# Kernel optimization log

Hardware: AMD Instinct MI355X
Metric: run time of the kernel (lower is better)

Reference implementation:

```python
import jax, jax.numpy as jnp
import numpy as np

N_SRC = 8192
N_DST = 8192
E = 524288
D = 128
M = 64


def layer_norm(x, g, b, eps=1e-5):
    mu = x.mean(-1, keepdims=True)
    var = ((x - mu) ** 2).mean(-1, keepdims=True)
    return (x - mu) * jax.lax.rsqrt(var + eps) * g + b


def setup_inputs() -> dict:
    key = jax.random.key(0)
    ks = jax.random.split(key, 32)

    def p(k, shape, s=0.02):
        return jax.random.normal(k, shape, jnp.float32) * s

    inp = {
        "src_embed": jax.random.normal(ks[0], (N_SRC, D), jnp.float32),
        "dst_embed": jax.random.normal(ks[1], (N_DST, D), jnp.float32),
        "v_s2d": jax.random.normal(ks[2], (E, M), jnp.float32),
        "v_d2s": jax.random.normal(ks[3], (E, M), jnp.float32),
        "e_s2d_dst": jax.random.randint(ks[4], (E,), 0, N_DST, jnp.int32),
        "e_d2s_dst": jax.random.randint(ks[5], (E,), 0, N_SRC, jnp.int32),
        # node transforms
        "W_src": p(ks[6], (D, D)), "b_src": jnp.zeros((D,), jnp.float32),
        "W_dst": p(ks[7], (D, D)), "b_dst": jnp.zeros((D,), jnp.float32),
        # edge-message transforms
        "W_sm": p(ks[8], (M, D)), "b_sm": jnp.zeros((D,), jnp.float32),
        "W_dm": p(ks[9], (M, D)), "b_dm": jnp.zeros((D,), jnp.float32),
        # apply_row: LNLayer (Linear+LayerNorm) then Linear
        "row_W1": p(ks[10], (D, D)), "row_b1": jnp.zeros((D,), jnp.float32),
        "row_g": jnp.ones((D,), jnp.float32), "row_beta": jnp.zeros((D,), jnp.float32),
        "row_W2": p(ks[11], (D, D)), "row_b2": jnp.zeros((D,), jnp.float32),
        # apply_col
        "col_W1": p(ks[12], (D, D)), "col_b1": jnp.zeros((D,), jnp.float32),
        "col_g": jnp.ones((D,), jnp.float32), "col_beta": jnp.zeros((D,), jnp.float32),
        "col_W2": p(ks[13], (D, D)), "col_b2": jnp.zeros((D,), jnp.float32),
    }
    return inp


def reference(src_embed, dst_embed, v_s2d, v_d2s, e_s2d_dst, e_d2s_dst,
              W_src, b_src, W_dst, b_dst, W_sm, b_sm, W_dm, b_dm,
              row_W1, row_b1, row_g, row_beta, row_W2, row_b2,
              col_W1, col_b1, col_g, col_beta, col_W2, col_b2):
    # node transforms: h[ntype]
    h_src = src_embed @ W_src + b_src          # [N_src, D]
    h_dst = dst_embed @ W_dst + b_dst          # [N_dst, D]
    # edge message transforms
    msg_s2d = v_s2d @ W_sm + b_sm              # [E, D]
    msg_d2s = v_d2s @ W_dm + b_dm              # [E, D]
    # message = h[dst-of-edge] * msg, scatter-sum onto destination nodes
    out_dst = jax.ops.segment_sum(h_dst[e_s2d_dst] * msg_s2d, e_s2d_dst,
                                  num_segments=N_DST)   # src2dst -> dst nodes
    out_src = jax.ops.segment_sum(h_src[e_d2s_dst] * msg_d2s, e_d2s_dst,
                                  num_segments=N_SRC)   # dst2src -> src nodes
    # residual apply: x + Linear(LayerNorm(Linear(out)))
    row = src_embed + (layer_norm(out_src @ row_W1 + row_b1, row_g, row_beta) @ row_W2 + row_b2)
    col = dst_embed + (layer_norm(out_dst @ col_W1 + col_b1, col_g, col_beta) @ col_W2 + col_b2)
    return row, col
```

## Files before the change

### kernel.cpp

```cpp
#include <hip/hip_runtime.h>


#define DEV __device__ __forceinline__

typedef __bf16 bf16x8 __attribute__((ext_vector_type(8)));
typedef unsigned short u16x8 __attribute__((ext_vector_type(8)));
typedef float f32x4 __attribute__((ext_vector_type(4)));

constexpr int N_NODES = 8192;
constexpr int NUM_E   = 524288;
constexpr int D       = 128;
constexpr int M       = 64;

DEV unsigned short f2bf(float f) {
    unsigned int x = __float_as_uint(f);
    unsigned int r = (x + 0x7fffu + ((x >> 16) & 1u)) >> 16;
    return (unsigned short)r;
}
DEV bf16x8 load8(const unsigned short* p) {
    return *reinterpret_cast<const bf16x8*>(p);
}
DEV bf16x8 cvt8(const float* p) {
    union { u16x8 u; bf16x8 b; } cv;
#pragma unroll
    for (int i = 0; i < 8; ++i) cv.u[i] = f2bf(p[i]);
    return cv.b;
}
DEV f32x4 mfma16(bf16x8 a, bf16x8 b, f32x4 c) {
    return __builtin_amdgcn_mfma_f32_16x16x32_bf16(a, b, c, 0, 0, 0);
}

__global__ __launch_bounds__(256) void hist_k(const int* __restrict__ i0,
                                              const int* __restrict__ i1,
                                              int* __restrict__ counts) {
    int t = blockIdx.x * 256 + threadIdx.x;
    int base = 0;
    const int4* p = (const int4*)i0;
    if (t >= NUM_E / 4) { p = (const int4*)i1; base = N_NODES; t -= NUM_E / 4; }
    int4 e = p[t];
    atomicAdd(counts + base + (e.x & (N_NODES - 1)), 1);
    atomicAdd(counts + base + (e.y & (N_NODES - 1)), 1);
    atomicAdd(counts + base + (e.z & (N_NODES - 1)), 1);
    atomicAdd(counts + base + (e.w & (N_NODES - 1)), 1);
}

__global__ __launch_bounds__(256) void scan_k(const int* __restrict__ counts,
                                              int* __restrict__ offsets,
                                              int* __restrict__ cursors) {
    __shared__ int part[256];
    int t = threadIdx.x;
    int dir = blockIdx.x;
    const int* c = counts + dir * N_NODES;
    int* off = offsets + dir * (N_NODES + 1);
    int* cur = cursors + dir * N_NODES;
    int local[32];
    int s = 0;
#pragma unroll
    for (int i = 0; i < 32; ++i) { int v = c[t * 32 + i]; local[i] = s; s += v; }
    part[t] = s;
    __syncthreads();
    for (int dd = 1; dd < 256; dd <<= 1) {
        int w = (t >= dd) ? part[t - dd] : 0;
        __syncthreads();
        part[t] += w;
        __syncthreads();
    }
    int base = part[t] - s;
#pragma unroll
    for (int i = 0; i < 32; ++i) { int o = base + local[i]; off[t * 32 + i] = o; cur[t * 32 + i] = o; }
    if (t == 255) off[N_NODES] = part[255];
}

__global__ __launch_bounds__(256) void scatter_k(const int* __restrict__ i0,
                                                 const int* __restrict__ i1,
                                                 int* __restrict__ cursors,
                                                 int* __restrict__ csr) {
    int t = blockIdx.x * 256 + threadIdx.x;
    int dir = 0;
    if (t >= NUM_E / 4) { dir = 1; t -= NUM_E / 4; }
    const int4* idx = (const int4*)(dir ? i1 : i0);
    int4 nn = idx[t];
    int* cur = cursors + dir * N_NODES;
    int* c = csr + dir * NUM_E;
    int e = t * 4;
    c[atomicAdd(cur + (nn.x & (N_NODES - 1)), 1)] = e;
    c[atomicAdd(cur + (nn.y & (N_NODES - 1)), 1)] = e + 1;
    c[atomicAdd(cur + (nn.z & (N_NODES - 1)), 1)] = e + 2;
    c[atomicAdd(cur + (nn.w & (N_NODES - 1)), 1)] = e + 3;
}

struct TransArgs {
    const float* src[8];
    unsigned short* dst[8];
    int K[8];
};
__global__ __launch_bounds__(256) void transpose_k(TransArgs ta) {
    int b = blockIdx.x;
    const float* s = ta.src[b];
    unsigned short* d = ta.dst[b];
    int K = ta.K[b];
    int total = K << 7;
    for (int i = threadIdx.x; i < total; i += 256) {
        int k = i >> 7, n = i & 127;
        d[n * K + k] = f2bf(s[i]);
    }
}

__global__ __launch_bounds__(256) void gather_k(const float* __restrict__ v,
                                                const int* __restrict__ off,
                                                const int* __restrict__ cs,
                                                unsigned short* __restrict__ Ab) {
    int n = (blockIdx.x * 256 + threadIdx.x) >> 6;
    int lane = threadIdx.x & 63;
    const int f16 = lane & 15;
    const int g = lane >> 4;
    int j0 = off[n], j1 = off[n + 1];
    f32x4 acc = {0.f, 0.f, 0.f, 0.f};

    int nfull = (j1 - j0) >> 4;
    int j = j0;
    if (nfull > 0) {
        int idx0 = cs[j + g], idx1 = cs[j + g + 4];
        int idx2 = cs[j + g + 8], idx3 = cs[j + g + 12];
        for (int it = 0; it < nfull; ++it) {
            int jn = j + 16;
            int p0 = 0, p1 = 0, p2 = 0, p3 = 0;
            if ((it + 1) < nfull) {
                p0 = cs[jn + g];
                p1 = cs[jn + g + 4];
                p2 = cs[jn + g + 8];
                p3 = cs[jn + g + 12];
            }
            f32x4 d0 = *(const f32x4*)(v + (size_t)idx0 * M + f16 * 4);
            f32x4 d1 = *(const f32x4*)(v + (size_t)idx1 * M + f16 * 4);
            f32x4 d2 = *(const f32x4*)(v + (size_t)idx2 * M + f16 * 4);
            f32x4 d3 = *(const f32x4*)(v + (size_t)idx3 * M + f16 * 4);
            acc += d0; acc += d1; acc += d2; acc += d3;
            idx0 = p0; idx1 = p1; idx2 = p2; idx3 = p3;
            j = jn;
        }
    }
    for (; j < j1; j += 4) {
        int e = j + g;
        if (e < j1) acc += *(const f32x4*)(v + (size_t)cs[e] * M + f16 * 4);
    }
#pragma unroll
    for (int i = 0; i < 4; ++i) {
        acc[i] += __shfl_xor(acc[i], 16, 64);
        acc[i] += __shfl_xor(acc[i], 32, 64);
    }
    if (g == 0) {
        union { unsigned short u[4]; unsigned long long ll; } w;
#pragma unroll
        for (int i = 0; i < 4; ++i) w.u[i] = f2bf(acc[i]);
        *reinterpret_cast<unsigned long long*>(Ab + (size_t)n * M + f16 * 4) = w.ll;
    }
}

struct SideArgs {
    const float* X;
    const unsigned short* Wnode_t;
    const float* bnode;
    const unsigned short* Abf;
    const int* counts;
    const unsigned short* Wmsg_t;
    const float* bmsg;
    const unsigned short* W1_t;
    const float* b1;
    const float* g;
    const float* beta;
    const unsigned short* W2_t;
    const float* b2;
    float* out;
};

__global__ __launch_bounds__(256) void apply_k(SideArgs A0, SideArgs A1) {
    const int side = blockIdx.x >> 9;
    const SideArgs& a = side ? A1 : A0;
    const int grp = blockIdx.x & 511;
    const int nb = grp * 16;
    const int w = threadIdx.x >> 6;
    const int lane = threadIdx.x & 63;
    const int m = lane & 15;
    const int quad = lane >> 4;

    __shared__ __align__(16) unsigned short sP[16 * 136];
    __shared__ float part_s[4][16], part_sq[4][16];

    bf16x8 af[4];
#pragma unroll
    for (int ks = 0; ks < 4; ++ks)
        af[ks] = cvt8(a.X + (size_t)(nb + m) * D + ks * 32 + quad * 8);
    f32x4 acc_h[2] = {{0.f, 0.f, 0.f, 0.f}, {0.f, 0.f, 0.f, 0.f}};
#pragma unroll
    for (int i = 0; i < 2; ++i) {
        int dt = 2 * w + i;
#pragma unroll
        for (int ks = 0; ks < 4; ++ks) {
            bf16x8 bfr = load8(a.Wnode_t + (size_t)(dt * 16 + m) * D + ks * 32 + quad * 8);
            acc_h[i] = mfma16(af[ks], bfr, acc_h[i]);
        }
    }
    bf16x8 at[2];
#pragma unroll
    for (int ks = 0; ks < 2; ++ks)
        at[ks] = load8(a.Abf + (size_t)(nb + m) * M + ks * 32 + quad * 8);
    f32x4 acc_t[2] = {{0.f, 0.f, 0.f, 0.f}, {0.f, 0.f, 0.f, 0.f}};
#pragma unroll
    for (int i = 0; i < 2; ++i) {
        int dt = 2 * w + i;
#pragma unroll
        for (int ks = 0; ks < 2; ++ks) {
            bf16x8 bfr = load8(a.Wmsg_t + (size_t)(dt * 16 + m) * M + ks * 32 + quad * 8);
            acc_t[i] = mfma16(at[ks], bfr, acc_t[i]);
        }
    }
    {
        float cnt_f[4];
#pragma unroll
        for (int r = 0; r < 4; ++r) cnt_f[r] = (float)a.counts[nb + quad * 4 + r];
#pragma unroll
        for (int i = 0; i < 2; ++i) {
            int dt = 2 * w + i;
            float bn = a.bnode[dt * 16 + m];
            float bm = a.bmsg[dt * 16 + m];
#pragma unroll
            for (int r = 0; r < 4; ++r) {
                float hv = acc_h[i][r] + bn;
                float tv = acc_t[i][r] + cnt_f[r] * bm;
                sP[(quad * 4 + r) * 136 + dt * 16 + m] = f2bf(hv * tv);
            }
        }
    }
    __syncthreads();
    bf16x8 au[4];
#pragma unroll
    for (int ks = 0; ks < 4; ++ks)
        au[ks] = load8(sP + m * 136 + ks * 32 + quad * 8);
    f32x4 acc_u[2] = {{0.f, 0.f, 0.f, 0.f}, {0.f, 0.f, 0.f, 0.f}};
#pragma unroll
    for (int i = 0; i < 2; ++i) {
        int dt = 2 * w + i;
#pragma unroll
        for (int ks = 0; ks < 4; ++ks) {
            bf16x8 bfr = load8(a.W1_t + (size_t)(dt * 16 + m) * D + ks * 32 + quad * 8);
            acc_u[i] = mfma16(au[ks], bfr, acc_u[i]);
        }
    }
    float g_f[2], beta_f[2];
#pragma unroll
    for (int i = 0; i < 2; ++i) {
        int dt = 2 * w + i;
        float b1v = a.b1[dt * 16 + m];
        g_f[i] = a.g[dt * 16 + m];
        beta_f[i] = a.beta[dt * 16 + m];
#pragma unroll
        for (int r = 0; r < 4; ++r) acc_u[i][r] += b1v;
    }
    float s[4], sq[4];
#pragma unroll
    for (int r = 0; r < 4; ++r) { s[r] = 0.f; sq[r] = 0.f; }
#pragma unroll
    for (int i = 0; i < 2; ++i)
#pragma unroll
        for (int r = 0; r < 4; ++r) { float u = acc_u[i][r]; s[r] += u; sq[r] += u * u; }
#pragma unroll
    for (int off = 1; off < 16; off <<= 1) {
#pragma unroll
        for (int r = 0; r < 4; ++r) {
            s[r] += __shfl_xor(s[r], off, 64);
            sq[r] += __shfl_xor(sq[r], off, 64);
        }
    }
    if (m == 0) {
#pragma unroll
        for (int r = 0; r < 4; ++r) {
            part_s[w][quad * 4 + r] = s[r];
            part_sq[w][quad * 4 + r] = sq[r];
        }
    }
    __syncthreads();
    float mu[4], rstd[4];
#pragma unroll
    for (int r = 0; r < 4; ++r) {
        int node = quad * 4 + r;
        float S = part_s[0][node] + part_s[1][node] + part_s[2][node] + part_s[3][node];
        float SQ = part_sq[0][node] + part_sq[1][node] + part_sq[2][node] + part_sq[3][node];
        mu[r] = S * (1.0f / 128.0f);
        float var = SQ * (1.0f / 128.0f) - mu[r] * mu[r];
        rstd[r] = rsqrtf(fmaxf(var, 0.f) + 1e-5f);
    }
#pragma unroll
    for (int i = 0; i < 2; ++i) {
        int dt = 2 * w + i;
#pragma unroll
        for (int r = 0; r < 4; ++r) {
            float ln = (acc_u[i][r] - mu[r]) * rstd[r] * g_f[i] + beta_f[i];
            sP[(quad * 4 + r) * 136 + dt * 16 + m] = f2bf(ln);
        }
    }
    __syncthreads();
    bf16x8 ay[4];
#pragma unroll
    for (int ks = 0; ks < 4; ++ks)
        ay[ks] = load8(sP + m * 136 + ks * 32 + quad * 8);
    f32x4 acc_y[2] = {{0.f, 0.f, 0.f, 0.f}, {0.f, 0.f, 0.f, 0.f}};
#pragma unroll
    for (int i = 0; i < 2; ++i) {
        int dt = 2 * w + i;
#pragma unroll
        for (int ks = 0; ks < 4; ++ks) {
            bf16x8 bfr = load8(a.W2_t + (size_t)(dt * 16 + m) * D + ks * 32 + quad * 8);
            acc_y[i] = mfma16(ay[ks], bfr, acc_y[i]);
        }
    }
#pragma unroll
    for (int i = 0; i < 2; ++i) {
        int dt = 2 * w + i;
        float b2v = a.b2[dt * 16 + m];
#pragma unroll
        for (int r = 0; r < 4; ++r) {
            int node = nb + quad * 4 + r;
            int d = dt * 16 + m;
            float xv = a.X[(size_t)node * D + d];
            a.out[(size_t)node * D + d] = acc_y[i][r] + b2v + xv;
        }
    }
}

extern "C" void kernel_launch(void* const* d_in, const int* in_sizes, int n_in,
                              void* d_out, int out_size, void* d_ws, size_t ws_size,
                              hipStream_t stream) {
    const float* src_embed = (const float*)d_in[0];
    const float* dst_embed = (const float*)d_in[1];
    const float* v_s2d = (const float*)d_in[2];
    const float* v_d2s = (const float*)d_in[3];
    const int* e_s2d = (const int*)d_in[4];
    const int* e_d2s = (const int*)d_in[5];
    const float* W_src = (const float*)d_in[6];
    const float* b_src = (const float*)d_in[7];
    const float* W_dst = (const float*)d_in[8];
    const float* b_dst = (const float*)d_in[9];
    const float* W_sm = (const float*)d_in[10];
    const float* b_sm = (const float*)d_in[11];
    const float* W_dm = (const float*)d_in[12];
    const float* b_dm = (const float*)d_in[13];
    const float* row_W1 = (const float*)d_in[14];
    const float* row_b1 = (const float*)d_in[15];
    const float* row_g = (const float*)d_in[16];
    const float* row_beta = (const float*)d_in[17];
    const float* row_W2 = (const float*)d_in[18];
    const float* row_b2 = (const float*)d_in[19];
    const float* col_W1 = (const float*)d_in[20];
    const float* col_b1 = (const float*)d_in[21];
    const float* col_g = (const float*)d_in[22];
    const float* col_beta = (const float*)d_in[23];
    const float* col_W2 = (const float*)d_in[24];
    const float* col_b2 = (const float*)d_in[25];
    float* out = (float*)d_out;

    char* ws = (char*)d_ws;
    int* counts = (int*)(ws + 0);
    int* offsets = (int*)(ws + 65536);
    int* cursors = (int*)(ws + 131328);
    unsigned short* Wt = (unsigned short*)(ws + 197120);
    unsigned short* Abf = (unsigned short*)(ws + 426752);
    int* csr = (int*)(out + (size_t)N_NODES * D);

    TransArgs ta;
    const float* srcs[8] = {W_src, W_dst, W_sm, W_dm, row_W1, row_W2, col_W1, col_W2};
    int Ks[8] = {128, 128, 64, 64, 128, 128, 128, 128};
    int offs[8] = {0, 16384, 32768, 40960, 49152, 65536, 81920, 98304};
    for (int i = 0; i < 8; ++i) { ta.src[i] = srcs[i]; ta.dst[i] = Wt + offs[i]; ta.K[i] = Ks[i]; }
    transpose_k<<<8, 256, 0, stream>>>(ta);

    hipMemsetAsync(counts, 0, 2 * N_NODES * sizeof(int), stream);
    hist_k<<<(2 * NUM_E / 4) / 256, 256, 0, stream>>>(e_s2d, e_d2s, counts);
    scan_k<<<2, 256, 0, stream>>>(counts, offsets, cursors);
    scatter_k<<<(2 * NUM_E / 4) / 256, 256, 0, stream>>>(e_s2d, e_d2s, cursors, csr);

    gather_k<<<(N_NODES * 64) / 256, 256, 0, stream>>>(
        v_s2d, offsets, csr, Abf);
    gather_k<<<(N_NODES * 64) / 256, 256, 0, stream>>>(
        v_d2s, offsets + (N_NODES + 1), csr + NUM_E, Abf + (size_t)N_NODES * M);

    SideArgs rowA = {src_embed, Wt + 0, b_src, Abf + (size_t)N_NODES * M, counts + N_NODES,
                     Wt + 40960, b_dm, Wt + 49152, row_b1, row_g, row_beta, Wt + 65536, row_b2,
                     out};
    SideArgs colA = {dst_embed, Wt + 16384, b_dst, Abf, counts,
                     Wt + 32768, b_sm, Wt + 81920, col_b1, col_g, col_beta, Wt + 98304, col_b2,
                     out + (size_t)N_NODES * D};
    apply_k<<<1024, 256, 0, stream>>>(rowA, colA);
}
```

Measured before the change: 492.1 us.

## Replicate histogram counters to cut atomic contention and merge gather launches

The histogram and scatter cursors are split into 16 replicas chosen by block index, so concurrent atomics on the same node go to different addresses. The scan kernel sums the replicas, writes per-node totals, and builds per-replica cursor bases. The counts memset is folded into the transpose kernel through extra zeroing blocks, and the two gather launches become one. In exchange the scan does more serial work in only two blocks, and the workspace grows to about 2 MB.

```diff
diff --git a/kernel.cpp b/kernel.cpp
--- a/kernel.cpp
+++ b/kernel.cpp
@@ -11,6 +11,7 @@
 constexpr int NUM_E   = 524288;
 constexpr int D       = 128;
 constexpr int M       = 64;
+constexpr int R       = 16;
 
 DEV unsigned short f2bf(float f) {
     unsigned int x = __float_as_uint(f);
@@ -30,13 +31,39 @@
     return __builtin_amdgcn_mfma_f32_16x16x32_bf16(a, b, c, 0, 0, 0);
 }
 
+struct TransArgs {
+    const float* src[8];
+    unsigned short* dst[8];
+    int K[8];
+};
+__global__ __launch_bounds__(256) void transpose_k(TransArgs ta, int* __restrict__ counts) {
+    int b = blockIdx.x;
+    if (b >= 8) {
+        int z = b - 8;
+        int4 zero = {0, 0, 0, 0};
+        int4* p = reinterpret_cast<int4*>(counts) + (size_t)z * 2048 + threadIdx.x;
+#pragma unroll
+        for (int q = 0; q < 8; ++q) p[q * 256] = zero;
+        return;
+    }
+    const float* s = ta.src[b];
+    unsigned short* d = ta.dst[b];
+    int K = ta.K[b];
+    int total = K << 7;
+    for (int i = threadIdx.x; i < total; i += 256) {
+        int k = i >> 7, n = i & 127;
+        d[n * K + k] = f2bf(s[i]);
+    }
+}
+
 __global__ __launch_bounds__(256) void hist_k(const int* __restrict__ i0,
                                               const int* __restrict__ i1,
                                               int* __restrict__ counts) {
     int t = blockIdx.x * 256 + threadIdx.x;
-    int base = 0;
+    int rep = blockIdx.x & (R - 1);
+    int base = rep * N_NODES;
     const int4* p = (const int4*)i0;
-    if (t >= NUM_E / 4) { p = (const int4*)i1; base = N_NODES; t -= NUM_E / 4; }
+    if (t >= NUM_E / 4) { p = (const int4*)i1; base += R * N_NODES; t -= NUM_E / 4; }
     int4 e = p[t];
     atomicAdd(counts + base + (e.x & (N_NODES - 1)), 1);
     atomicAdd(counts + base + (e.y & (N_NODES - 1)), 1);
@@ -46,17 +73,32 @@
 
 __global__ __launch_bounds__(256) void scan_k(const int* __restrict__ counts,
                                               int* __restrict__ offsets,
-                                              int* __restrict__ cursors) {
+                                              int* __restrict__ cursors,
+                                              int* __restrict__ tot) {
     __shared__ int part[256];
     int t = threadIdx.x;
     int dir = blockIdx.x;
-    const int* c = counts + dir * N_NODES;
+    const int* c = counts + (size_t)dir * R * N_NODES;
     int* off = offsets + dir * (N_NODES + 1);
-    int* cur = cursors + dir * N_NODES;
+    int* cur = cursors + (size_t)dir * R * N_NODES;
+    int* tt = tot + dir * N_NODES;
+
+    int sums[32];
+#pragma unroll
+    for (int i = 0; i < 32; ++i) sums[i] = 0;
+    for (int r = 0; r < R; ++r) {
+        const int4* p = (const int4*)(c + r * N_NODES + t * 32);
+#pragma unroll
+        for (int q = 0; q < 8; ++q) {
+            int4 v = p[q];
+            sums[q * 4 + 0] += v.x; sums[q * 4 + 1] += v.y;
+            sums[q * 4 + 2] += v.z; sums[q * 4 + 3] += v.w;
+        }
+    }
     int local[32];
     int s = 0;
 #pragma unroll
-    for (int i = 0; i < 32; ++i) { int v = c[t * 32 + i]; local[i] = s; s += v; }
+    for (int i = 0; i < 32; ++i) { local[i] = s; s += sums[i]; }
     part[t] = s;
     __syncthreads();
     for (int dd = 1; dd < 256; dd <<= 1) {
@@ -67,8 +109,28 @@
     }
     int base = part[t] - s;
 #pragma unroll
-    for (int i = 0; i < 32; ++i) { int o = base + local[i]; off[t * 32 + i] = o; cur[t * 32 + i] = o; }
+    for (int i = 0; i < 32; ++i) {
+        off[t * 32 + i] = base + local[i];
+        tt[t * 32 + i] = sums[i];
+    }
     if (t == 255) off[N_NODES] = part[255];
+    int run[32];
+#pragma unroll
+    for (int i = 0; i < 32; ++i) run[i] = base + local[i];
+    for (int r = 0; r < R; ++r) {
+        const int4* p = (const int4*)(c + r * N_NODES + t * 32);
+        int4* cp = (int4*)(cur + r * N_NODES + t * 32);
+#pragma unroll
+        for (int q = 0; q < 8; ++q) {
+            int4 v = p[q];
+            int4 w;
+            w.x = run[q * 4 + 0]; w.y = run[q * 4 + 1];
+            w.z = run[q * 4 + 2]; w.w = run[q * 4 + 3];
+            cp[q] = w;
+            run[q * 4 + 0] += v.x; run[q * 4 + 1] += v.y;
+            run[q * 4 + 2] += v.z; run[q * 4 + 3] += v.w;
+        }
+    }
 }
 
 __global__ __launch_bounds__(256) void scatter_k(const int* __restrict__ i0,
@@ -76,11 +138,12 @@
                                                  int* __restrict__ cursors,
                                                  int* __restrict__ csr) {
     int t = blockIdx.x * 256 + threadIdx.x;
+    int rep = blockIdx.x & (R - 1);
     int dir = 0;
     if (t >= NUM_E / 4) { dir = 1; t -= NUM_E / 4; }
     const int4* idx = (const int4*)(dir ? i1 : i0);
     int4 nn = idx[t];
-    int* cur = cursors + dir * N_NODES;
+    int* cur = cursors + (size_t)dir * R * N_NODES + rep * N_NODES;
     int* c = csr + dir * NUM_E;
     int e = t * 4;
     c[atomicAdd(cur + (nn.x & (N_NODES - 1)), 1)] = e;
@@ -89,28 +152,19 @@
     c[atomicAdd(cur + (nn.w & (N_NODES - 1)), 1)] = e + 3;
 }
 
-struct TransArgs {
-    const float* src[8];
-    unsigned short* dst[8];
-    int K[8];
-};
-__global__ __launch_bounds__(256) void transpose_k(TransArgs ta) {
-    int b = blockIdx.x;
-    const float* s = ta.src[b];
-    unsigned short* d = ta.dst[b];
-    int K = ta.K[b];
-    int total = K << 7;
-    for (int i = threadIdx.x; i < total; i += 256) {
-        int k = i >> 7, n = i & 127;
-        d[n * K + k] = f2bf(s[i]);
-    }
-}
-
-__global__ __launch_bounds__(256) void gather_k(const float* __restrict__ v,
-                                                const int* __restrict__ off,
-                                                const int* __restrict__ cs,
+__global__ __launch_bounds__(256) void gather_k(const float* __restrict__ v0,
+                                                const float* __restrict__ v1,
+                                                const int* __restrict__ offsets,
+                                                const int* __restrict__ csr,
                                                 unsigned short* __restrict__ Ab) {
-    int n = (blockIdx.x * 256 + threadIdx.x) >> 6;
+    int gw = (blockIdx.x * 256 + threadIdx.x) >> 6;
+    int dir = gw >> 13;
+    int n = gw & (N_NODES - 1);
+    const float* v = dir ? v1 : v0;
+    const int* off = offsets + dir * (N_NODES + 1);
+    const int* cs = csr + dir * NUM_E;
+    unsigned short* A = Ab + (size_t)dir * N_NODES * M;
+
     int lane = threadIdx.x & 63;
     const int f16 = lane & 15;
     const int g = lane >> 4;
@@ -153,7 +207,7 @@
         union { unsigned short u[4]; unsigned long long ll; } w;
 #pragma unroll
         for (int i = 0; i < 4; ++i) w.u[i] = f2bf(acc[i]);
-        *reinterpret_cast<unsigned long long*>(Ab + (size_t)n * M + f16 * 4) = w.ll;
+        *reinterpret_cast<unsigned long long*>(A + (size_t)n * M + f16 * 4) = w.ll;
     }
 }
 
@@ -361,10 +415,11 @@
 
     char* ws = (char*)d_ws;
     int* counts = (int*)(ws + 0);
-    int* offsets = (int*)(ws + 65536);
-    int* cursors = (int*)(ws + 131328);
-    unsigned short* Wt = (unsigned short*)(ws + 197120);
-    unsigned short* Abf = (unsigned short*)(ws + 426752);
+    int* offsets = (int*)(ws + 1048576);
+    int* cursors = (int*)(ws + 1114368);
+    int* tot = (int*)(ws + 2162944);
+    unsigned short* Wt = (unsigned short*)(ws + 2228480);
+    unsigned short* Abf = (unsigned short*)(ws + 2457856);
     int* csr = (int*)(out + (size_t)N_NODES * D);
 
     TransArgs ta;
@@ -372,22 +427,19 @@
     int Ks[8] = {128, 128, 64, 64, 128, 128, 128, 128};
     int offs[8] = {0, 16384, 32768, 40960, 49152, 65536, 81920, 98304};
     for (int i = 0; i < 8; ++i) { ta.src[i] = srcs[i]; ta.dst[i] = Wt + offs[i]; ta.K[i] = Ks[i]; }
-    transpose_k<<<8, 256, 0, stream>>>(ta);
-
-    hipMemsetAsync(counts, 0, 2 * N_NODES * sizeof(int), stream);
+    transpose_k<<<40, 256, 0, stream>>>(ta, counts);
+
     hist_k<<<(2 * NUM_E / 4) / 256, 256, 0, stream>>>(e_s2d, e_d2s, counts);
-    scan_k<<<2, 256, 0, stream>>>(counts, offsets, cursors);
+    scan_k<<<2, 256, 0, stream>>>(counts, offsets, cursors, tot);
     scatter_k<<<(2 * NUM_E / 4) / 256, 256, 0, stream>>>(e_s2d, e_d2s, cursors, csr);
 
-    gather_k<<<(N_NODES * 64) / 256, 256, 0, stream>>>(
-        v_s2d, offsets, csr, Abf);
-    gather_k<<<(N_NODES * 64) / 256, 256, 0, stream>>>(
-        v_d2s, offsets + (N_NODES + 1), csr + NUM_E, Abf + (size_t)N_NODES * M);
-
-    SideArgs rowA = {src_embed, Wt + 0, b_src, Abf + (size_t)N_NODES * M, counts + N_NODES,
+    gather_k<<<(2 * N_NODES * 64) / 256, 256, 0, stream>>>(
+        v_s2d, v_d2s, offsets, csr, Abf);
+
+    SideArgs rowA = {src_embed, Wt + 0, b_src, Abf + (size_t)N_NODES * M, tot + N_NODES,
                      Wt + 40960, b_dm, Wt + 49152, row_b1, row_g, row_beta, Wt + 65536, row_b2,
                      out};
-    SideArgs colA = {dst_embed, Wt + 16384, b_dst, Abf, counts,
+    SideArgs colA = {dst_embed, Wt + 16384, b_dst, Abf, tot,
                      Wt + 32768, b_sm, Wt + 81920, col_b1, col_g, col_beta, Wt + 98304, col_b2,
                      out + (size_t)N_NODES * D};
     apply_k<<<1024, 256, 0, stream>>>(rowA, colA);
```

After: 524.2 us. 6.5% more time.
